# Performance work log

Hardware: AMD Instinct MI355X
Metric: run time of the kernel (lower is better)

The kernel has to match this reference:

```python
import jax, jax.numpy as jnp
import numpy as np

B, C, H, W = 16, 128, 224, 224
G = 4  # granularities[0]


def setup_inputs() -> dict:
    key = jax.random.key(0)
    kx, kp = jax.random.split(key)
    x = jax.random.normal(kx, (B, C, H, W), dtype=jnp.float32)
    # one independent permutation of the G*G block positions per batch element
    perm = jax.vmap(lambda k: jax.random.permutation(k, G * G))(
        jax.random.split(kp, B)
    ).astype(jnp.int32)  # [B, G*G]
    return {"x": x, "perm": perm}


def reference(x, perm):
    # H, W divisible by G -> no interpolation branch.
    b, c, h, w = x.shape
    bh, bw = h // G, w // G
    # [B,C,H,W] -> [B, G*G, C, bh, bw]: block (i,j) at flat index i*G+j
    blocks = (
        x.reshape(b, c, G, bh, G, bw)
        .transpose(0, 2, 4, 1, 3, 5)
        .reshape(b, G * G, c, bh, bw)
    )
    # torch loop does shuffled[b, perm[b, k]] = blocks[b, k] (scatter).
    # Gather form: shuffled[b, i] = blocks[b, argsort(perm)[b, i]].
    inv = jnp.argsort(perm, axis=1)  # [B, G*G]
    shuffled = jnp.take_along_axis(blocks, inv[:, :, None, None, None], axis=1)
    out = (
        shuffled.reshape(b, G, G, c, bh, bw)
        .transpose(0, 3, 1, 4, 2, 5)
        .reshape(b, c, h, w)
    )
    return out
```

## Files before the change

kernel.cpp:

```cpp
#include <hip/hip_runtime.h>

constexpr int B = 16, C = 128, H = 224, W = 224, G = 4;
constexpr int BH = H / G;
constexpr int BW4 = (W / G) / 4;
constexpr int W4 = W / 4;
constexpr int TOTAL4 = B * C * H * W4;

__global__ __launch_bounds__(256) void block_shuffle_kernel(
    const float4* __restrict__ x, const int* __restrict__ perm,
    float4* __restrict__ out) {
  int idx = blockIdx.x * 256 + threadIdx.x;
  if (idx >= TOTAL4) return;

  int w4 = idx % W4;
  int t  = idx / W4;
  int h  = t % H;
  int bc = t / H;
  int b  = bc / C;

  int si = h / BH;
  int y  = h - si * BH;
  int sj = w4 / BW4;
  int x4 = w4 - sj * BW4;

  int p  = perm[b * (G * G) + si * G + sj];
  int oi = p >> 2;
  int oj = p & 3;

  int oidx = (bc * H + oi * BH + y) * W4 + oj * BW4 + x4;
  out[oidx] = x[idx];
}

extern "C" void kernel_launch(void* const* d_in, const int* in_sizes, int n_in,
                              void* d_out, int out_size, void* d_ws, size_t ws_size,
                              hipStream_t stream) {
  const float4* x = (const float4*)d_in[0];
  const int* perm = (const int*)d_in[1];
  float4* out = (float4*)d_out;

  constexpr int kBlock = 256;
  constexpr int kGrid = (TOTAL4 + kBlock - 1) / kBlock;
  block_shuffle_kernel<<<kGrid, kBlock, 0, stream>>>(x, perm, out);
}
```

Measured before the change: 676.8 us.

## Stage rows in LDS so block shuffle writes whole output rows

Each workgroup now loads, for one batch, one intra-block row offset and eight channels, the four matching image rows into shared memory. It builds the inverse permutation in LDS and writes complete output rows with the shuffled blocks gathered from the tile. Before, each thread wrote float4s to permuted locations, so writes only formed 224-byte contiguous segments; now reads and writes both cover full contiguous rows. The cost is a ~28KB LDS tile per workgroup, which limits occupancy, plus a barrier between the load and store phases.

```diff
diff --git a/kernel.cpp b/kernel.cpp
--- a/kernel.cpp
+++ b/kernel.cpp
@@ -4,31 +4,60 @@
 constexpr int BH = H / G;
 constexpr int BW4 = (W / G) / 4;
 constexpr int W4 = W / 4;
-constexpr int TOTAL4 = B * C * H * W4;
+constexpr int CCHUNK = 8;
+constexpr int QROW = G * W4;
+constexpr int NF4 = CCHUNK * QROW;
+constexpr int THREADS = 256;
+constexpr int PER_THREAD = NF4 / THREADS;
+constexpr int NWG = B * BH * (C / CCHUNK);
 
-__global__ __launch_bounds__(256) void block_shuffle_kernel(
+__global__ __launch_bounds__(256) void block_shuffle_lds(
     const float4* __restrict__ x, const int* __restrict__ perm,
     float4* __restrict__ out) {
-  int idx = blockIdx.x * 256 + threadIdx.x;
-  if (idx >= TOTAL4) return;
+  __shared__ float4 tile[NF4];
+  __shared__ int inv[G * G];
 
-  int w4 = idx % W4;
-  int t  = idx / W4;
-  int h  = t % H;
-  int bc = t / H;
-  int b  = bc / C;
+  int wg = blockIdx.x;
+  int cblk = wg % (C / CCHUNK);
+  int t    = wg / (C / CCHUNK);
+  int y    = t % BH;
+  int b    = t / BH;
+  int c0   = cblk * CCHUNK;
 
-  int si = h / BH;
-  int y  = h - si * BH;
-  int sj = w4 / BW4;
-  int x4 = w4 - sj * BW4;
+  int tid = threadIdx.x;
+  if (tid < G * G) {
+    int p = perm[b * (G * G) + tid];
+    inv[p] = tid;
+  }
 
-  int p  = perm[b * (G * G) + si * G + sj];
-  int oi = p >> 2;
-  int oj = p & 3;
+  int basebc = (b * C + c0) * H;
 
-  int oidx = (bc * H + oi * BH + y) * W4 + oj * BW4 + x4;
-  out[oidx] = x[idx];
+#pragma unroll
+  for (int p = 0; p < PER_THREAD; ++p) {
+    int j  = tid + p * THREADS;
+    int cc = j / QROW;
+    int w  = j - cc * QROW;
+    int si = w / W4;
+    int w4 = w - si * W4;
+    tile[j] = x[(basebc + cc * H + si * BH + y) * W4 + w4];
+  }
+  __syncthreads();
+
+#pragma unroll
+  for (int p = 0; p < PER_THREAD; ++p) {
+    int j   = tid + p * THREADS;
+    int cc  = j / QROW;
+    int w   = j - cc * QROW;
+    int oi  = w / W4;
+    int w4  = w - oi * W4;
+    int oj  = w4 / BW4;
+    int x4  = w4 - oj * BW4;
+    int src = inv[oi * G + oj];
+    int si  = src >> 2;
+    int sj  = src & 3;
+    float4 v = tile[cc * QROW + si * W4 + sj * BW4 + x4];
+    out[(basebc + cc * H + oi * BH + y) * W4 + w4] = v;
+  }
 }
 
 extern "C" void kernel_launch(void* const* d_in, const int* in_sizes, int n_in,
@@ -37,8 +66,5 @@
   const float4* x = (const float4*)d_in[0];
   const int* perm = (const int*)d_in[1];
   float4* out = (float4*)d_out;
-
-  constexpr int kBlock = 256;
-  constexpr int kGrid = (TOTAL4 + kBlock - 1) / kBlock;
-  block_shuffle_kernel<<<kGrid, kBlock, 0, stream>>>(x, perm, out);
+  block_shuffle_lds<<<NWG, THREADS, 0, stream>>>(x, perm, out);
 }
```

After: 646.4 us. -4.5%, faster.
